# Optimization experiments

Hardware: AMD Instinct MI355X
Metric: run time of the kernel (lower is better)

Reference implementation:

```python
import jax, jax.numpy as jnp
import numpy as np

N_EMBD = 1024
N_HEADS = 16
HEAD_SIZE = N_EMBD // N_HEADS
B, T = 1, 4096
LN_EPS = 1e-5


def setup_inputs() -> dict:
    key = jax.random.key(0)
    ks = jax.random.split(key, 12)
    s = lambda fan_in: 1.0 / np.sqrt(fan_in)
    return {
        "x": jax.random.normal(ks[0], (B, T, N_EMBD), dtype=jnp.float32),
        # per-head Q/K/V projections (no bias), stacked over heads: [H, C, hd]
        "Wq": jax.random.normal(ks[1], (N_HEADS, N_EMBD, HEAD_SIZE), dtype=jnp.float32) * s(N_EMBD),
        "Wk": jax.random.normal(ks[2], (N_HEADS, N_EMBD, HEAD_SIZE), dtype=jnp.float32) * s(N_EMBD),
        "Wv": jax.random.normal(ks[3], (N_HEADS, N_EMBD, HEAD_SIZE), dtype=jnp.float32) * s(N_EMBD),
        # output projection (with bias)
        "Wp": jax.random.normal(ks[4], (N_EMBD, N_EMBD), dtype=jnp.float32) * s(N_EMBD),
        "bp": jnp.zeros((N_EMBD,), dtype=jnp.float32),
        # FFN: Linear(C, 4C) -> ReLU -> Linear(4C, C)
        "W1": jax.random.normal(ks[5], (N_EMBD, 4 * N_EMBD), dtype=jnp.float32) * s(N_EMBD),
        "b1": jnp.zeros((4 * N_EMBD,), dtype=jnp.float32),
        "W2": jax.random.normal(ks[6], (4 * N_EMBD, N_EMBD), dtype=jnp.float32) * s(4 * N_EMBD),
        "b2": jnp.zeros((N_EMBD,), dtype=jnp.float32),
        # LayerNorms
        "g1": jnp.ones((N_EMBD,), dtype=jnp.float32),
        "be1": jnp.zeros((N_EMBD,), dtype=jnp.float32),
        "g2": jnp.ones((N_EMBD,), dtype=jnp.float32),
        "be2": jnp.zeros((N_EMBD,), dtype=jnp.float32),
    }


def _layernorm(x, gamma, beta):
    mu = jnp.mean(x, axis=-1, keepdims=True)
    var = jnp.mean(jnp.square(x - mu), axis=-1, keepdims=True)
    return (x - mu) * jax.lax.rsqrt(var + LN_EPS) * gamma + beta


def _block(x, Wq, Wk, Wv, Wp, bp, W1, b1, W2, b2, g1, be1, g2, be2):
    Bn, Tn, C = x.shape
    h = _layernorm(x, g1, be1)
    # per-head projections: [B, H, T, hd]
    q = jnp.einsum("btc,hcd->bhtd", h, Wq)
    k = jnp.einsum("btc,hcd->bhtd", h, Wk)
    v = jnp.einsum("btc,hcd->bhtd", h, Wv)
    # NOTE: original scales by C**-0.5 where C = n_embd (not head_size)
    scores = jnp.einsum("bhtd,bhsd->bhts", q, k) * (C ** -0.5)
    causal = jnp.tril(jnp.ones((Tn, Tn), dtype=bool))
    scores = jnp.where(causal, scores, -jnp.inf)
    w = jax.nn.softmax(scores, axis=-1)
    attn = jnp.einsum("bhts,bhsd->bhtd", w, v)
    # concat heads: [B, T, H*hd] = [B, T, C]
    attn = attn.transpose(0, 2, 1, 3).reshape(Bn, Tn, C)
    x = x + attn @ Wp + bp
    h2 = _layernorm(x, g2, be2)
    ff = jax.nn.relu(h2 @ W1 + b1) @ W2 + b2
    return x + ff


def reference(x, Wq, Wk, Wv, Wp, bp, W1, b1, W2, b2, g1, be1, g2, be2):
    return _block(x, Wq, Wk, Wv, Wp, bp, W1, b1, W2, b2, g1, be1, g2, be2)
```

## Files before the change

### kernel.cpp

```cpp
#include <hip/hip_runtime.h>
#include <cstdint>

typedef __attribute__((ext_vector_type(8))) short bf16x8;
typedef __attribute__((ext_vector_type(4))) float f32x4;
typedef __attribute__((ext_vector_type(16))) float f32x16;
typedef __attribute__((ext_vector_type(4))) unsigned int u32x4;

__device__ __forceinline__ short f2b(float f) {
  unsigned u = __builtin_bit_cast(unsigned, f);
  unsigned r = (u + 0x7fffu + ((u >> 16) & 1u)) >> 16;
  return (short)(unsigned short)r;
}
__device__ __forceinline__ float b2f(short s) {
  unsigned u = ((unsigned)(unsigned short)s) << 16;
  return __builtin_bit_cast(float, u);
}

__device__ __forceinline__ void gload16(void* lds_dst, const void* gsrc) {
  __builtin_amdgcn_global_load_lds(
      (const __attribute__((address_space(1))) void*)gsrc,
      (__attribute__((address_space(3))) void*)lds_dst, 16, 0, 0);
}

__device__ __forceinline__ unsigned cvtpk(float a, float b) {
  unsigned r;
  asm("v_cvt_pk_bf16_f32 %0, %1, %2" : "=v"(r) : "v"(a), "v"(b));
  return r;
}
__device__ __forceinline__ unsigned shflx32(unsigned v) {
  return (unsigned)__shfl_xor((int)v, 32);
}
__device__ __forceinline__ float exp2x(float x) {
  float r;
  asm("v_exp_f32 %0, %1" : "=v"(r) : "v"(x));
  return r;
}

__device__ __forceinline__ void plswap(unsigned &a, unsigned &b) {
#if __has_builtin(__builtin_amdgcn_permlane32_swap)
  auto r = __builtin_amdgcn_permlane32_swap((int)a, (int)b, false, false);
  a = (unsigned)r[0];
  b = (unsigned)r[1];
#else
  const bool lo = ((threadIdx.x & 63) < 32);
  unsigned ax = shflx32(a), bx = shflx32(b);
  unsigned na = lo ? a : bx;
  unsigned nb = lo ? ax : b;
  a = na; b = nb;
#endif
}

__global__ __launch_bounds__(256)
void prep_all(const float* __restrict__ Wq, const float* __restrict__ Wk,
              const float* __restrict__ Wv, const float* __restrict__ Wp,
              const float* __restrict__ W1, const float* __restrict__ W2,
              const float* __restrict__ x, const float* __restrict__ g1,
              const float* __restrict__ be1,
              short* __restrict__ WqkvT, short* __restrict__ WpT,
              short* __restrict__ W1T, short* __restrict__ W2T,
              short* __restrict__ hbuf)
{
  const int id = blockIdx.x;
  if (id < 12288) {
    __shared__ float tl[32][33];
    const int tx = threadIdx.x & 31;
    const int ty = threadIdx.x >> 5;
    if (id < 3072) {
      const int which = id >> 10;
      const int rem = id & 1023;
      const int head = rem >> 6;
      const int tile = rem & 63;
      const int tc = tile >> 1, td = tile & 1;
      const float* src = (which == 0 ? Wq : which == 1 ? Wk : Wv) + (long)head * 65536;
#pragma unroll
      for (int i2 = 0; i2 < 4; ++i2) {
        int i = ty + i2 * 8;
        tl[i][tx] = src[(long)(tc * 32 + i) * 64 + td * 32 + tx];
      }
      __syncthreads();
      const long base = (long)which * 1024 + head * 64 + td * 32;
#pragma unroll
      for (int i2 = 0; i2 < 4; ++i2) {
        int i = ty + i2 * 8;
        WqkvT[(base + i) * 1024 + tc * 32 + tx] = f2b(tl[tx][i]);
      }
    } else {
      const float* src;
      short* dst;
      int rows, cols, bx, by;
      if (id < 4096) {
        src = Wp; dst = WpT; rows = 1024; cols = 1024;
        const int k = id - 3072; bx = k & 31; by = k >> 5;
      } else if (id < 8192) {
        src = W1; dst = W1T; rows = 1024; cols = 4096;
        const int k = id - 4096; bx = k & 127; by = k >> 7;
      } else {
        src = W2; dst = W2T; rows = 4096; cols = 1024;
        const int k = id - 8192; bx = k & 31; by = k >> 5;
      }
#pragma unroll
      for (int i2 = 0; i2 < 4; ++i2) {
        int i = ty + i2 * 8;
        tl[i][tx] = src[(long)(by * 32 + i) * cols + bx * 32 + tx];
      }
      __syncthreads();
#pragma unroll
      for (int i2 = 0; i2 < 4; ++i2) {
        int i = ty + i2 * 8;
        dst[(long)(bx * 32 + i) * rows + by * 32 + tx] = f2b(tl[tx][i]);
      }
    }
  } else {
    const int row = id - 12288;
    const int t = threadIdx.x;
    const float4 v = ((const float4*)(x + (long)row * 1024))[t];
    float s = v.x + v.y + v.z + v.w;
    float ss = v.x * v.x + v.y * v.y + v.z * v.z + v.w * v.w;
#pragma unroll
    for (int off = 1; off < 64; off <<= 1) {
      s += __shfl_xor(s, off);
      ss += __shfl_xor(ss, off);
    }
    __shared__ float red[8];
    const int wave = t >> 6, lane = t & 63;
    if (lane == 0) { red[wave] = s; red[4 + wave] = ss; }
    __syncthreads();
    s = red[0] + red[1] + red[2] + red[3];
    ss = red[4] + red[5] + red[6] + red[7];
    const float mu = s * (1.f / 1024.f);
    const float rstd = rsqrtf(ss * (1.f / 1024.f) - mu * mu + 1e-5f);
    const float4 gv = ((const float4*)g1)[t];
    const float4 bv = ((const float4*)be1)[t];
    short4 ov;
    ov.x = f2b((v.x - mu) * rstd * gv.x + bv.x);
    ov.y = f2b((v.y - mu) * rstd * gv.y + bv.y);
    ov.z = f2b((v.z - mu) * rstd * gv.z + bv.z);
    ov.w = f2b((v.w - mu) * rstd * gv.w + bv.w);
    *(short4*)(hbuf + (long)row * 1024 + t * 4) = ov;
  }
}

__global__ void vtrans(const short* __restrict__ qkv, short* __restrict__ Vt)
{
  __shared__ short tl[32][33];
  const int t0 = blockIdx.x * 32;
  const int c0 = blockIdx.y * 32;
  const int head = c0 >> 6, d0 = c0 & 63;
  const int tx = threadIdx.x;
#pragma unroll
  for (int i2 = 0; i2 < 4; ++i2) {
    int i = threadIdx.y + i2 * 8;
    tl[i][tx] = qkv[(long)(t0 + i) * 3072 + 2048 + c0 + tx];
  }
  __syncthreads();
#pragma unroll
  for (int i2 = 0; i2 < 4; ++i2) {
    int i = threadIdx.y + i2 * 8;
    Vt[(long)head * 262144 + (long)(d0 + i) * 4096 + t0 + tx] = tl[tx][i];
  }
}

__global__ __launch_bounds__(256)
void layernorm_bf16(const float* __restrict__ x, const float* __restrict__ g,
                    const float* __restrict__ be, short* __restrict__ outp)
{
  const int row = blockIdx.x;
  const int t = threadIdx.x;
  const float4 v = ((const float4*)(x + (long)row * 1024))[t];
  float s = v.x + v.y + v.z + v.w;
  float ss = v.x * v.x + v.y * v.y + v.z * v.z + v.w * v.w;
#pragma unroll
  for (int off = 1; off < 64; off <<= 1) {
    s += __shfl_xor(s, off);
    ss += __shfl_xor(ss, off);
  }
  __shared__ float red[8];
  const int wave = t >> 6, lane = t & 63;
  if (lane == 0) { red[wave] = s; red[4 + wave] = ss; }
  __syncthreads();
  s = red[0] + red[1] + red[2] + red[3];
  ss = red[4] + red[5] + red[6] + red[7];
  const float mu = s * (1.f / 1024.f);
  const float rstd = rsqrtf(ss * (1.f / 1024.f) - mu * mu + 1e-5f);
  const float4 gv = ((const float4*)g)[t];
  const float4 bv = ((const float4*)be)[t];
  short4 ov;
  ov.x = f2b((v.x - mu) * rstd * gv.x + bv.x);
  ov.y = f2b((v.y - mu) * rstd * gv.y + bv.y);
  ov.z = f2b((v.z - mu) * rstd * gv.z + bv.z);
  ov.w = f2b((v.w - mu) * rstd * gv.w + bv.w);
  *(short4*)(outp + (long)row * 1024 + t * 4) = ov;
}

template<int EPI>
__global__ __launch_bounds__(512, 2)
void gemm128(const short* __restrict__ A, const short* __restrict__ Bt,
             int N, int K, int NT,
             short* __restrict__ Cb, float* __restrict__ Cf,
             const float* __restrict__ bias, const float* __restrict__ resid)
{
  __shared__ __align__(16) short As[2 * 8192];
  __shared__ __align__(16) short Bs[2 * 8192];
  const int tid = threadIdx.x;
  const int lane = tid & 63;
  const int wave = tid >> 6;
  const int wm = wave >> 2;
  const int wn = wave & 3;
  const int l15 = lane & 15, lg = lane >> 4;

  const int nwg = gridDim.x * gridDim.y;
  const int lin = blockIdx.y * gridDim.x + blockIdx.x;
  const int swz = (lin & 7) * (nwg >> 3) + (lin >> 3);
  const long m0 = (long)(swz / gridDim.x) * 128;
  const long n0 = (long)(swz % gridDim.x) * 128;

  const int rloc = lane >> 3;
  const int csrc = (lane & 7) ^ rloc;
  const short* Ag = A + (m0 + wave * 8 + rloc) * K + csrc * 8;
  const short* Bg = Bt + (n0 + wave * 8 + rloc) * K + csrc * 8;
  const int wbase = wave * 512;

  f32x4 acc[4][2] = {};

#define STAGE128(buf, kt)                                                     \
  do {                                                                        \
    gload16(As + (buf) * 8192 + wbase, Ag + (kt));                            \
    gload16(As + (buf) * 8192 + 4096 + wbase, Ag + (long)64 * K + (kt));      \
    gload16(Bs + (buf) * 8192 + wbase, Bg + (kt));                            \
    gload16(Bs + (buf) * 8192 + 4096 + wbase, Bg + (long)64 * K + (kt));      \
  } while (0)

  STAGE128(0, 0);
  STAGE128(1, 64);
  asm volatile("s_waitcnt vmcnt(4)" ::: "memory");
  __builtin_amdgcn_sched_barrier(0);
  __builtin_amdgcn_s_barrier();
  __builtin_amdgcn_sched_barrier(0);

  const int cA = l15 & 7;
  for (int t = 0; t < NT; ++t) {
    const char* Ab = (const char*)(As + (t & 1) * 8192);
    const char* Bb = (const char*)(Bs + (t & 1) * 8192);
#pragma unroll
    for (int kk = 0; kk < 2; ++kk) {
      bf16x8 af[4], bk[2];
#pragma unroll
      for (int mi = 0; mi < 4; ++mi)
        af[mi] = *(const bf16x8*)(Ab + (wm * 64 + mi * 16 + l15) * 128 + 16 * ((kk * 4 + lg) ^ cA));
#pragma unroll
      for (int ni = 0; ni < 2; ++ni)
        bk[ni] = *(const bf16x8*)(Bb + (wn * 32 + ni * 16 + l15) * 128 + 16 * ((kk * 4 + lg) ^ cA));
      __builtin_amdgcn_s_setprio(1);
#pragma unroll
      for (int mi = 0; mi < 4; ++mi)
#pragma unroll
        for (int ni = 0; ni < 2; ++ni)
          acc[mi][ni] = __builtin_amdgcn_mfma_f32_16x16x32_bf16(af[mi], bk[ni], acc[mi][ni], 0, 0, 0);
      __builtin_amdgcn_s_setprio(0);
    }
    if (t == NT - 1) break;
    __builtin_amdgcn_s_barrier();
    __builtin_amdgcn_sched_barrier(0);
    if (t + 2 < NT) {
      STAGE128(t & 1, (long)(t + 2) * 64);
      asm volatile("s_waitcnt vmcnt(4)" ::: "memory");
    } else {
      asm volatile("s_waitcnt vmcnt(0)" ::: "memory");
    }
    __builtin_amdgcn_sched_barrier(0);
    __builtin_amdgcn_s_barrier();
    __builtin_amdgcn_sched_barrier(0);
  }
#undef STAGE128

#pragma unroll
  for (int mi = 0; mi < 4; ++mi) {
#pragma unroll
    for (int ni = 0; ni < 2; ++ni) {
      const long col = n0 + wn * 32 + ni * 16 + l15;
#pragma unroll
      for (int r = 0; r < 4; ++r) {
        const long row = m0 + wm * 64 + mi * 16 + lg * 4 + r;
        const long idx = row * N + col;
        float v = acc[mi][ni][r];
        if (EPI == 0) {
          Cb[idx] = f2b(v);
        } else {
          Cf[idx] = v + bias[col] + resid[idx];
        }
      }
    }
  }
}

__device__ __forceinline__ void stage256(short* AsB, short* BsB,
                                         const short* Ag, const short* Bg,
                                         long kt, int K, int ldsoff)
{
#pragma unroll
  for (int p = 0; p < 4; ++p)
    gload16(AsB + p * 4096 + ldsoff, Ag + (long)p * 64 * K + kt);
#pragma unroll
  for (int p = 0; p < 4; ++p)
    gload16(BsB + p * 4096 + ldsoff, Bg + (long)p * 64 * K + kt);
}

template<int EPI>
__global__ __launch_bounds__(512, 2)
void gemm256(const short* __restrict__ A, const short* __restrict__ Bt,
             int N, int K, int NT,
             short* __restrict__ Cb, const float* __restrict__ bias)
{
  __shared__ __align__(16) short As[2 * 16384];
  __shared__ __align__(16) short Bs[2 * 16384];
  const int tid = threadIdx.x;
  const int lane = tid & 63;
  const int wave = tid >> 6;
  const int wm = wave >> 2;
  const int wn = wave & 3;
  const int l15 = lane & 15, lg = lane >> 4;

  const int nwg = gridDim.x * gridDim.y;
  const int lin = blockIdx.y * gridDim.x + blockIdx.x;
  const int swz = (lin & 7) * (nwg >> 3) + (lin >> 3);
  const long m0 = (long)(swz / gridDim.x) * 256;
  const long n0 = (long)(swz % gridDim.x) * 256;

  const int trow = tid >> 3;
  const int csrc = (tid & 7) ^ (trow & 7);
  const short* Ag = A + (m0 + trow) * K + csrc * 8;
  const short* Bg = Bt + (n0 + trow) * K + csrc * 8;
  const int ldsoff = wave * 512;

  f32x4 acc[8][4] = {};

  stage256(As, Bs, Ag, Bg, 0, K, ldsoff);
  asm volatile("s_waitcnt vmcnt(0)" ::: "memory");
  __builtin_amdgcn_sched_barrier(0);
  __builtin_amdgcn_s_barrier();
  __builtin_amdgcn_sched_barrier(0);

  const int cA = l15 & 7;
  for (int t = 0; t < NT; ++t) {
    const char* Ab = (const char*)(As + (t & 1) * 16384);
    const char* Bb = (const char*)(Bs + (t & 1) * 16384);
    short* Asn = As + ((t + 1) & 1) * 16384;
    short* Bsn = Bs + ((t + 1) & 1) * 16384;
    const bool more = (t + 1 < NT);
    const long ktn = (long)(t + 1) * 64;
    bf16x8 bk[4];
#pragma unroll
    for (int ph = 0; ph < 4; ++ph) {
      const int kk = ph >> 1;
      const int mh = (ph & 1) * 4;
      bf16x8 af[4];
#pragma unroll
      for (int mi = 0; mi < 4; ++mi)
        af[mi] = *(const bf16x8*)(Ab + (wm * 128 + (mh + mi) * 16 + l15) * 128 + 16 * ((kk * 4 + lg) ^ cA));
      if ((ph & 1) == 0) {
#pragma unroll
        for (int ni = 0; ni < 4; ++ni)
          bk[ni] = *(const bf16x8*)(Bb + (wn * 64 + ni * 16 + l15) * 128 + 16 * ((kk * 4 + lg) ^ cA));
      }
      if (more && ph == 0) {
#pragma unroll
        for (int p = 0; p < 4; ++p)
          gload16(Asn + p * 4096 + ldsoff, Ag + (long)p * 64 * K + ktn);
      }
      if (more && ph == 1) {
#pragma unroll
        for (int p = 0; p < 4; ++p)
          gload16(Bsn + p * 4096 + ldsoff, Bg + (long)p * 64 * K + ktn);
      }
      __builtin_amdgcn_s_barrier();
      asm volatile("s_waitcnt lgkmcnt(0)" ::: "memory");
      __builtin_amdgcn_sched_barrier(0);
      __builtin_amdgcn_s_setprio(1);
#pragma unroll
      for (int mi = 0; mi < 4; ++mi)
#pragma unroll
        for (int ni = 0; ni < 4; ++ni)
          acc[mh + mi][ni] = __builtin_amdgcn_mfma_f32_16x16x32_bf16(af[mi], bk[ni], acc[mh + mi][ni], 0, 0, 0);
      __builtin_amdgcn_s_setprio(0);
      if (ph == 3 && more) {
        asm volatile("s_waitcnt vmcnt(0)" ::: "memory");
        __builtin_amdgcn_sched_barrier(0);
      }
      __builtin_amdgcn_s_barrier();
      __builtin_amdgcn_sched_barrier(0);
    }
  }

#pragma unroll
  for (int mi = 0; mi < 8; ++mi) {
#pragma unroll
    for (int ni = 0; ni < 4; ++ni) {
      const long col = n0 + wn * 64 + ni * 16 + l15;
      const float bb = (EPI == 2) ? bias[col] : 0.f;
#pragma unroll
      for (int r = 0; r < 4; ++r) {
        const long row = m0 + wm * 128 + mi * 16 + lg * 4 + r;
        float v = acc[mi][ni][r];
        if (EPI == 2) { v += bb; v = v > 0.f ? v : 0.f; }
        Cb[row * N + col] = f2b(v);
      }
    }
  }
}

__device__ __forceinline__ void stage_k32(short* lds, const short* gRowBase)
{
  const int lane = threadIdx.x & 63;
  const int rloc = lane >> 3;
  const int cs = (lane & 7) ^ rloc;
#pragma unroll
  for (int p = 0; p < 4; ++p)
    gload16(lds + p * 512, gRowBase + (long)(p * 8 + rloc) * 3072 + cs * 8);
}
__device__ __forceinline__ void stage_v32(short* lds, const short* vHeadBase, int t0)
{
  const int lane = threadIdx.x & 63;
  const int rloc = lane >> 3;
  const int cs = (lane & 7) ^ rloc;
#pragma unroll
  for (int p = 0; p < 4; ++p) {
    const int row = p * 8 + rloc;
    const int d = row + ((cs & 4) << 3);
    gload16(lds + p * 512, vHeadBase + (long)d * 4096 + t0 + (cs & 3) * 8);
  }
}

__global__ __launch_bounds__(256)
void attn_fwd4(const short* __restrict__ qkv, const short* __restrict__ Vt,
               short* __restrict__ outp)
{
  __shared__ __align__(16) short KV[4 * 8192];
  __shared__ __align__(16) short OB[64 * 64];
  __shared__ float lAll[64];

  const int tid = threadIdx.x;
  const int lane = tid & 63;
  const int wave = tid >> 6;
  const int wq = wave & 1;
  const int ks = wave >> 1;
  const int l31 = lane & 31;
  const int h = lane >> 5;
  const int rs = l31 & 7;

  const int id = blockIdx.x;
  const int head = ((id & 7) << 1) | (id >> 8);
  const int bx = (id >> 3) & 31;

  const short* Qg = qkv + head * 64;
  const short* Kg = qkv + 1024 + head * 64;
  const short* Vg = Vt + (long)head * 262144;

  short* Kw = KV + wave * 8192;

  bf16x8 onesf;
#pragma unroll
  for (int j = 0; j < 8; ++j) onesf[j] = (short)0x3F80;

  for (int ph = 0; ph < 2; ++ph) {
    const int qsuper = ph ? (63 - bx) : bx;
    const int q0 = qsuper * 64 + wq * 32;
    const int q = q0 + l31;
    const int nt = qsuper + 1;

    bf16x8 qf[4];
#pragma unroll
    for (int d = 0; d < 4; ++d) {
      bf16x8 tq = *(const bf16x8*)(Qg + (long)q * 3072 + d * 16 + h * 8);
#pragma unroll
      for (int j = 0; j < 8; ++j) tq[j] = f2b(b2f(tq[j]) * (0.03125f * 1.44269504f));
      qf[d] = tq;
    }

    f32x16 o0 = {}, o1 = {}, lacc = {};

    stage_k32(Kw, Kg + (long)(ks * 32) * 3072);
    stage_v32(Kw + 2048, Vg, ks * 32);
    if (nt > 1) {
      stage_k32(Kw + 4096, Kg + (long)(64 + ks * 32) * 3072);
      stage_v32(Kw + 4096 + 2048, Vg, 64 + ks * 32);
    }

    for (int t = 0; t < nt; ++t) {
      if (t + 1 < nt) {
        asm volatile("s_waitcnt vmcnt(8)" ::: "memory");
      } else {
        asm volatile("s_waitcnt vmcnt(0)" ::: "memory");
      }
      __builtin_amdgcn_sched_barrier(0);
      const char* Kb = (const char*)(Kw + (t & 1) * 4096);
      const char* Vb = Kb + 4096;
      const bf16x8 kf0 = *(const bf16x8*)(Kb + l31 * 128 + 16 * ((0 + h) ^ rs));
      const bf16x8 kf1 = *(const bf16x8*)(Kb + l31 * 128 + 16 * ((2 + h) ^ rs));
      const bf16x8 kf2 = *(const bf16x8*)(Kb + l31 * 128 + 16 * ((4 + h) ^ rs));
      const bf16x8 kf3 = *(const bf16x8*)(Kb + l31 * 128 + 16 * ((6 + h) ^ rs));
      const bf16x8 vf00 = *(const bf16x8*)(Vb + l31 * 128 + 16 * ((0 + h) ^ rs));
      const bf16x8 vf01 = *(const bf16x8*)(Vb + l31 * 128 + 16 * ((2 + h) ^ rs));
      const bf16x8 vf10 = *(const bf16x8*)(Vb + l31 * 128 + 16 * ((4 + h) ^ rs));
      const bf16x8 vf11 = *(const bf16x8*)(Vb + l31 * 128 + 16 * ((6 + h) ^ rs));
      asm volatile("s_waitcnt lgkmcnt(0)" ::: "memory");
      __builtin_amdgcn_sched_barrier(0);
      if (t + 2 < nt) {
        stage_k32(Kw + (t & 1) * 4096, Kg + (long)((t + 2) * 64 + ks * 32) * 3072);
        stage_v32(Kw + (t & 1) * 4096 + 2048, Vg, (t + 2) * 64 + ks * 32);
      }
      f32x16 s = {};
      __builtin_amdgcn_s_setprio(1);
      s = __builtin_amdgcn_mfma_f32_32x32x16_bf16(kf0, qf[0], s, 0, 0, 0);
      s = __builtin_amdgcn_mfma_f32_32x32x16_bf16(kf1, qf[1], s, 0, 0, 0);
      s = __builtin_amdgcn_mfma_f32_32x32x16_bf16(kf2, qf[2], s, 0, 0, 0);
      s = __builtin_amdgcn_mfma_f32_32x32x16_bf16(kf3, qf[3], s, 0, 0, 0);
      __builtin_amdgcn_s_setprio(0);
      if (t == qsuper) {
        const int kb0 = t * 64 + ks * 32 + 4 * h;
#pragma unroll
        for (int r = 0; r < 16; ++r) {
          const int k0 = kb0 + (r & 3) + 8 * (r >> 2);
          if (k0 > q) s[r] = -INFINITY;
        }
      }
#pragma unroll
      for (int r = 0; r < 16; ++r) s[r] = exp2x(s[r]);
      unsigned P0 = cvtpk(s[0], s[1]),   P1 = cvtpk(s[2], s[3]);
      unsigned P2 = cvtpk(s[4], s[5]),   P3 = cvtpk(s[6], s[7]);
      unsigned P4 = cvtpk(s[8], s[9]),   P5 = cvtpk(s[10], s[11]);
      unsigned P6 = cvtpk(s[12], s[13]), P7 = cvtpk(s[14], s[15]);
      plswap(P0, P2); plswap(P1, P3); plswap(P4, P6); plswap(P5, P7);
      u32x4 f0, f1;
      f0[0] = P0; f0[1] = P1; f0[2] = P2; f0[3] = P3;
      f1[0] = P4; f1[1] = P5; f1[2] = P6; f1[3] = P7;
      const bf16x8 pa0 = __builtin_bit_cast(bf16x8, f0);
      const bf16x8 pa1 = __builtin_bit_cast(bf16x8, f1);
      __builtin_amdgcn_s_setprio(1);
      o0 = __builtin_amdgcn_mfma_f32_32x32x16_bf16(pa0, vf00, o0, 0, 0, 0);
      o0 = __builtin_amdgcn_mfma_f32_32x32x16_bf16(pa1, vf01, o0, 0, 0, 0);
      o1 = __builtin_amdgcn_mfma_f32_32x32x16_bf16(pa0, vf10, o1, 0, 0, 0);
      o1 = __builtin_amdgcn_mfma_f32_32x32x16_bf16(pa1, vf11, o1, 0, 0, 0);
      lacc = __builtin_amdgcn_mfma_f32_32x32x16_bf16(pa0, onesf, lacc, 0, 0, 0);
      lacc = __builtin_amdgcn_mfma_f32_32x32x16_bf16(pa1, onesf, lacc, 0, 0, 0);
      __builtin_amdgcn_s_setprio(0);
    }

    if (ks == 1) {
#pragma unroll
      for (int r = 0; r < 16; ++r) {
        const int qq = wq * 32 + (r & 3) + 8 * (r >> 2) + 4 * h;
        OB[qq * 64 + l31] = f2b(o0[r]);
        OB[qq * 64 + 32 + l31] = f2b(o1[r]);
      }
      if (l31 == 0) {
#pragma unroll
        for (int r = 0; r < 16; ++r) {
          const int qq = wq * 32 + (r & 3) + 8 * (r >> 2) + 4 * h;
          lAll[qq] = lacc[r];
        }
      }
    }
    __syncthreads();
    if (ks == 0) {
#pragma unroll
      for (int r = 0; r < 16; ++r) {
        const int qq = wq * 32 + (r & 3) + 8 * (r >> 2) + 4 * h;
        const float inv = 1.f / (lacc[r] + lAll[qq]);
        const long qr = (long)qsuper * 64 + qq;
        const float v0 = o0[r] + b2f(OB[qq * 64 + l31]);
        const float v1 = o1[r] + b2f(OB[qq * 64 + 32 + l31]);
        outp[qr * 1024 + head * 64 + l31] = f2b(v0 * inv);
        outp[qr * 1024 + head * 64 + 32 + l31] = f2b(v1 * inv);
      }
    }
    __syncthreads();
  }
}

extern "C" void kernel_launch(void* const* d_in, const int* in_sizes, int n_in,
                              void* d_out, int out_size, void* d_ws, size_t ws_size,
                              hipStream_t stream)
{
  (void)in_sizes; (void)n_in; (void)out_size; (void)ws_size;
  const float* x   = (const float*)d_in[0];
  const float* Wq  = (const float*)d_in[1];
  const float* Wk  = (const float*)d_in[2];
  const float* Wv  = (const float*)d_in[3];
  const float* Wp  = (const float*)d_in[4];
  const float* bp  = (const float*)d_in[5];
  const float* W1  = (const float*)d_in[6];
  const float* b1  = (const float*)d_in[7];
  const float* W2  = (const float*)d_in[8];
  const float* b2  = (const float*)d_in[9];
  const float* g1  = (const float*)d_in[10];
  const float* be1 = (const float*)d_in[11];
  const float* g2  = (const float*)d_in[12];
  const float* be2 = (const float*)d_in[13];
  float* out = (float*)d_out;

  char* ws = (char*)d_ws;
  const size_t MB = 1ull << 20;
  short* WqkvT = (short*)(ws + 0 * MB);
  short* WpT   = (short*)(ws + 6 * MB);
  short* W1T   = (short*)(ws + 8 * MB);
  short* W2T   = (short*)(ws + 16 * MB);
  short* hbuf  = (short*)(ws + 24 * MB);
  short* qkvb  = (short*)(ws + 32 * MB);
  short* attnb = (short*)(ws + 56 * MB);
  float* x1    = (float*)(ws + 64 * MB);
  short* Vtb   = (short*)(ws + 64 * MB);

  prep_all<<<16384, 256, 0, stream>>>(Wq, Wk, Wv, Wp, W1, W2, x, g1, be1,
                                      WqkvT, WpT, W1T, W2T, hbuf);
  gemm256<0><<<dim3(12, 16), 512, 0, stream>>>(hbuf, WqkvT, 3072, 1024, 16,
                                               qkvb, nullptr);
  vtrans<<<dim3(128, 32), dim3(32, 8), 0, stream>>>(qkvb, Vtb);
  attn_fwd4<<<512, 256, 0, stream>>>(qkvb, Vtb, attnb);
  gemm128<1><<<dim3(8, 32), 512, 0, stream>>>(attnb, WpT, 1024, 1024, 16,
                                              nullptr, x1, bp, x);
  layernorm_bf16<<<4096, 256, 0, stream>>>(x1, g2, be2, hbuf);
  gemm256<2><<<dim3(16, 16), 512, 0, stream>>>(hbuf, W1T, 4096, 1024, 16,
                                               qkvb, b1);
  gemm128<1><<<dim3(8, 32), 512, 0, stream>>>(qkvb, W2T, 1024, 4096, 64,
                                              nullptr, out, b2, x1);
}
```

Before: 248.5 us.

## Replace 256-tile GEMMs with 128-tile kernel and process two KV blocks per attention step

The 256x256-tile gemm256 kernel is removed. The QKV and FFN-up GEMMs now use gemm128, which gains a bias+ReLU epilogue (EPI==2), so those launches get four times as many smaller workgroups for better CU fill. The attention kernel is restructured to consume two 64-key blocks per iteration, with both halves of the LDS buffer refilled together and interleaved MFMA chains. This cuts the number of waits and iterations but changes the prefetch distance, which may expose more memory latency and raise register pressure.

Result: slower. 274.9 us (+10.7%).

```diff
diff --git a/kernel.cpp b/kernel.cpp
--- a/kernel.cpp
+++ b/kernel.cpp
@@ -278,6 +278,7 @@
 #pragma unroll
     for (int ni = 0; ni < 2; ++ni) {
       const long col = n0 + wn * 32 + ni * 16 + l15;
+      const float bb = (EPI == 2) ? bias[col] : 0.f;
 #pragma unroll
       for (int r = 0; r < 4; ++r) {
         const long row = m0 + wm * 64 + mi * 16 + lg * 4 + r;
@@ -285,124 +286,12 @@
         float v = acc[mi][ni][r];
         if (EPI == 0) {
           Cb[idx] = f2b(v);
+        } else if (EPI == 1) {
+          Cf[idx] = v + bias[col] + resid[idx];
         } else {
-          Cf[idx] = v + bias[col] + resid[idx];
+          v += bb;
+          Cb[idx] = f2b(v > 0.f ? v : 0.f);
         }
-      }
-    }
-  }
-}
-
-__device__ __forceinline__ void stage256(short* AsB, short* BsB,
-                                         const short* Ag, const short* Bg,
-                                         long kt, int K, int ldsoff)
-{
-#pragma unroll
-  for (int p = 0; p < 4; ++p)
-    gload16(AsB + p * 4096 + ldsoff, Ag + (long)p * 64 * K + kt);
-#pragma unroll
-  for (int p = 0; p < 4; ++p)
-    gload16(BsB + p * 4096 + ldsoff, Bg + (long)p * 64 * K + kt);
-}
-
-template<int EPI>
-__global__ __launch_bounds__(512, 2)
-void gemm256(const short* __restrict__ A, const short* __restrict__ Bt,
-             int N, int K, int NT,
-             short* __restrict__ Cb, const float* __restrict__ bias)
-{
-  __shared__ __align__(16) short As[2 * 16384];
-  __shared__ __align__(16) short Bs[2 * 16384];
-  const int tid = threadIdx.x;
-  const int lane = tid & 63;
-  const int wave = tid >> 6;
-  const int wm = wave >> 2;
-  const int wn = wave & 3;
-  const int l15 = lane & 15, lg = lane >> 4;
-
-  const int nwg = gridDim.x * gridDim.y;
-  const int lin = blockIdx.y * gridDim.x + blockIdx.x;
-  const int swz = (lin & 7) * (nwg >> 3) + (lin >> 3);
-  const long m0 = (long)(swz / gridDim.x) * 256;
-  const long n0 = (long)(swz % gridDim.x) * 256;
-
-  const int trow = tid >> 3;
-  const int csrc = (tid & 7) ^ (trow & 7);
-  const short* Ag = A + (m0 + trow) * K + csrc * 8;
-  const short* Bg = Bt + (n0 + trow) * K + csrc * 8;
-  const int ldsoff = wave * 512;
-
-  f32x4 acc[8][4] = {};
-
-  stage256(As, Bs, Ag, Bg, 0, K, ldsoff);
-  asm volatile("s_waitcnt vmcnt(0)" ::: "memory");
-  __builtin_amdgcn_sched_barrier(0);
-  __builtin_amdgcn_s_barrier();
-  __builtin_amdgcn_sched_barrier(0);
-
-  const int cA = l15 & 7;
-  for (int t = 0; t < NT; ++t) {
-    const char* Ab = (const char*)(As + (t & 1) * 16384);
-    const char* Bb = (const char*)(Bs + (t & 1) * 16384);
-    short* Asn = As + ((t + 1) & 1) * 16384;
-    short* Bsn = Bs + ((t + 1) & 1) * 16384;
-    const bool more = (t + 1 < NT);
-    const long ktn = (long)(t + 1) * 64;
-    bf16x8 bk[4];
-#pragma unroll
-    for (int ph = 0; ph < 4; ++ph) {
-      const int kk = ph >> 1;
-      const int mh = (ph & 1) * 4;
-      bf16x8 af[4];
-#pragma unroll
-      for (int mi = 0; mi < 4; ++mi)
-        af[mi] = *(const bf16x8*)(Ab + (wm * 128 + (mh + mi) * 16 + l15) * 128 + 16 * ((kk * 4 + lg) ^ cA));
-      if ((ph & 1) == 0) {
-#pragma unroll
-        for (int ni = 0; ni < 4; ++ni)
-          bk[ni] = *(const bf16x8*)(Bb + (wn * 64 + ni * 16 + l15) * 128 + 16 * ((kk * 4 + lg) ^ cA));
-      }
-      if (more && ph == 0) {
-#pragma unroll
-        for (int p = 0; p < 4; ++p)
-          gload16(Asn + p * 4096 + ldsoff, Ag + (long)p * 64 * K + ktn);
-      }
-      if (more && ph == 1) {
-#pragma unroll
-        for (int p = 0; p < 4; ++p)
-          gload16(Bsn + p * 4096 + ldsoff, Bg + (long)p * 64 * K + ktn);
-      }
-      __builtin_amdgcn_s_barrier();
-      asm volatile("s_waitcnt lgkmcnt(0)" ::: "memory");
-      __builtin_amdgcn_sched_barrier(0);
-      __builtin_amdgcn_s_setprio(1);
-#pragma unroll
-      for (int mi = 0; mi < 4; ++mi)
-#pragma unroll
-        for (int ni = 0; ni < 4; ++ni)
-          acc[mh + mi][ni] = __builtin_amdgcn_mfma_f32_16x16x32_bf16(af[mi], bk[ni], acc[mh + mi][ni], 0, 0, 0);
-      __builtin_amdgcn_s_setprio(0);
-      if (ph == 3 && more) {
-        asm volatile("s_waitcnt vmcnt(0)" ::: "memory");
-        __builtin_amdgcn_sched_barrier(0);
-      }
-      __builtin_amdgcn_s_barrier();
-      __builtin_amdgcn_sched_barrier(0);
-    }
-  }
-
-#pragma unroll
-  for (int mi = 0; mi < 8; ++mi) {
-#pragma unroll
-    for (int ni = 0; ni < 4; ++ni) {
-      const long col = n0 + wn * 64 + ni * 16 + l15;
-      const float bb = (EPI == 2) ? bias[col] : 0.f;
-#pragma unroll
-      for (int r = 0; r < 4; ++r) {
-        const long row = m0 + wm * 128 + mi * 16 + lg * 4 + r;
-        float v = acc[mi][ni][r];
-        if (EPI == 2) { v += bb; v = v > 0.f ? v : 0.f; }
-        Cb[row * N + col] = f2b(v);
       }
     }
   }
@@ -431,7 +320,7 @@
 }
 
 __global__ __launch_bounds__(256)
-void attn_fwd4(const short* __restrict__ qkv, const short* __restrict__ Vt,
+void attn_fwd5(const short* __restrict__ qkv, const short* __restrict__ Vt,
                short* __restrict__ outp)
 {
   __shared__ __align__(16) short KV[4 * 8192];
@@ -482,66 +371,152 @@
     stage_v32(Kw + 2048, Vg, ks * 32);
     if (nt > 1) {
       stage_k32(Kw + 4096, Kg + (long)(64 + ks * 32) * 3072);
-      stage_v32(Kw + 4096 + 2048, Vg, 64 + ks * 32);
-    }
-
-    for (int t = 0; t < nt; ++t) {
-      if (t + 1 < nt) {
-        asm volatile("s_waitcnt vmcnt(8)" ::: "memory");
-      } else {
-        asm volatile("s_waitcnt vmcnt(0)" ::: "memory");
-      }
+      stage_v32(Kw + 6144, Vg, 64 + ks * 32);
+    }
+
+    int t = 0;
+    for (; t + 1 < nt; t += 2) {
+      asm volatile("s_waitcnt vmcnt(0)" ::: "memory");
       __builtin_amdgcn_sched_barrier(0);
-      const char* Kb = (const char*)(Kw + (t & 1) * 4096);
-      const char* Vb = Kb + 4096;
-      const bf16x8 kf0 = *(const bf16x8*)(Kb + l31 * 128 + 16 * ((0 + h) ^ rs));
-      const bf16x8 kf1 = *(const bf16x8*)(Kb + l31 * 128 + 16 * ((2 + h) ^ rs));
-      const bf16x8 kf2 = *(const bf16x8*)(Kb + l31 * 128 + 16 * ((4 + h) ^ rs));
-      const bf16x8 kf3 = *(const bf16x8*)(Kb + l31 * 128 + 16 * ((6 + h) ^ rs));
-      const bf16x8 vf00 = *(const bf16x8*)(Vb + l31 * 128 + 16 * ((0 + h) ^ rs));
-      const bf16x8 vf01 = *(const bf16x8*)(Vb + l31 * 128 + 16 * ((2 + h) ^ rs));
-      const bf16x8 vf10 = *(const bf16x8*)(Vb + l31 * 128 + 16 * ((4 + h) ^ rs));
-      const bf16x8 vf11 = *(const bf16x8*)(Vb + l31 * 128 + 16 * ((6 + h) ^ rs));
+      const char* Kb0 = (const char*)Kw;
+      const char* Vb0 = Kb0 + 4096;
+      const char* Kb1 = Kb0 + 8192;
+      const char* Vb1 = Kb0 + 12288;
+      bf16x8 k0f[4], k1f[4], v0f[4], v1f[4];
+#pragma unroll
+      for (int c = 0; c < 4; ++c) {
+        k0f[c] = *(const bf16x8*)(Kb0 + l31 * 128 + 16 * ((2 * c + h) ^ rs));
+        k1f[c] = *(const bf16x8*)(Kb1 + l31 * 128 + 16 * ((2 * c + h) ^ rs));
+      }
+#pragma unroll
+      for (int c = 0; c < 4; ++c) {
+        v0f[c] = *(const bf16x8*)(Vb0 + l31 * 128 + 16 * ((2 * c + h) ^ rs));
+        v1f[c] = *(const bf16x8*)(Vb1 + l31 * 128 + 16 * ((2 * c + h) ^ rs));
+      }
       asm volatile("s_waitcnt lgkmcnt(0)" ::: "memory");
       __builtin_amdgcn_sched_barrier(0);
-      if (t + 2 < nt) {
-        stage_k32(Kw + (t & 1) * 4096, Kg + (long)((t + 2) * 64 + ks * 32) * 3072);
-        stage_v32(Kw + (t & 1) * 4096 + 2048, Vg, (t + 2) * 64 + ks * 32);
-      }
-      f32x16 s = {};
+      if (t + 3 < nt) {
+        stage_k32(Kw, Kg + (long)((t + 2) * 64 + ks * 32) * 3072);
+        stage_v32(Kw + 2048, Vg, (t + 2) * 64 + ks * 32);
+        stage_k32(Kw + 4096, Kg + (long)((t + 3) * 64 + ks * 32) * 3072);
+        stage_v32(Kw + 6144, Vg, (t + 3) * 64 + ks * 32);
+      } else if (t + 2 < nt) {
+        stage_k32(Kw, Kg + (long)((t + 2) * 64 + ks * 32) * 3072);
+        stage_v32(Kw + 2048, Vg, (t + 2) * 64 + ks * 32);
+      }
+      f32x16 sA = {}, sB = {};
       __builtin_amdgcn_s_setprio(1);
-      s = __builtin_amdgcn_mfma_f32_32x32x16_bf16(kf0, qf[0], s, 0, 0, 0);
-      s = __builtin_amdgcn_mfma_f32_32x32x16_bf16(kf1, qf[1], s, 0, 0, 0);
-      s = __builtin_amdgcn_mfma_f32_32x32x16_bf16(kf2, qf[2], s, 0, 0, 0);
-      s = __builtin_amdgcn_mfma_f32_32x32x16_bf16(kf3, qf[3], s, 0, 0, 0);
+      sA = __builtin_amdgcn_mfma_f32_32x32x16_bf16(k0f[0], qf[0], sA, 0, 0, 0);
+      sB = __builtin_amdgcn_mfma_f32_32x32x16_bf16(k1f[0], qf[0], sB, 0, 0, 0);
+      sA = __builtin_amdgcn_mfma_f32_32x32x16_bf16(k0f[1], qf[1], sA, 0, 0, 0);
+      sB = __builtin_amdgcn_mfma_f32_32x32x16_bf16(k1f[1], qf[1], sB, 0, 0, 0);
+      sA = __builtin_amdgcn_mfma_f32_32x32x16_bf16(k0f[2], qf[2], sA, 0, 0, 0);
+      sB = __builtin_amdgcn_mfma_f32_32x32x16_bf16(k1f[2], qf[2], sB, 0, 0, 0);
+      sA = __builtin_amdgcn_mfma_f32_32x32x16_bf16(k0f[3], qf[3], sA, 0, 0, 0);
+      sB = __builtin_amdgcn_mfma_f32_32x32x16_bf16(k1f[3], qf[3], sB, 0, 0, 0);
       __builtin_amdgcn_s_setprio(0);
       if (t == qsuper) {
         const int kb0 = t * 64 + ks * 32 + 4 * h;
 #pragma unroll
         for (int r = 0; r < 16; ++r) {
           const int k0 = kb0 + (r & 3) + 8 * (r >> 2);
-          if (k0 > q) s[r] = -INFINITY;
+          if (k0 > q) sA[r] = -INFINITY;
         }
       }
-#pragma unroll
-      for (int r = 0; r < 16; ++r) s[r] = exp2x(s[r]);
-      unsigned P0 = cvtpk(s[0], s[1]),   P1 = cvtpk(s[2], s[3]);
-      unsigned P2 = cvtpk(s[4], s[5]),   P3 = cvtpk(s[6], s[7]);
-      unsigned P4 = cvtpk(s[8], s[9]),   P5 = cvtpk(s[10], s[11]);
-      unsigned P6 = cvtpk(s[12], s[13]), P7 = cvtpk(s[14], s[15]);
-      plswap(P0, P2); plswap(P1, P3); plswap(P4, P6); plswap(P5, P7);
-      u32x4 f0, f1;
-      f0[0] = P0; f0[1] = P1; f0[2] = P2; f0[3] = P3;
-      f1[0] = P4; f1[1] = P5; f1[2] = P6; f1[3] = P7;
-      const bf16x8 pa0 = __builtin_bit_cast(bf16x8, f0);
-      const bf16x8 pa1 = __builtin_bit_cast(bf16x8, f1);
+      if (t + 1 == qsuper) {
+        const int kb1 = (t + 1) * 64 + ks * 32 + 4 * h;
+#pragma unroll
+        for (int r = 0; r < 16; ++r) {
+          const int k1 = kb1 + (r & 3) + 8 * (r >> 2);
+          if (k1 > q) sB[r] = -INFINITY;
+        }
+      }
+#pragma unroll
+      for (int r = 0; r < 16; ++r) {
+        sA[r] = exp2x(sA[r]);
+        sB[r] = exp2x(sB[r]);
+      }
+      unsigned A0 = cvtpk(sA[0], sA[1]),   A1 = cvtpk(sA[2], sA[3]);
+      unsigned A2 = cvtpk(sA[4], sA[5]),   A3 = cvtpk(sA[6], sA[7]);
+      unsigned A4 = cvtpk(sA[8], sA[9]),   A5 = cvtpk(sA[10], sA[11]);
+      unsigned A6 = cvtpk(sA[12], sA[13]), A7 = cvtpk(sA[14], sA[15]);
+      unsigned B0 = cvtpk(sB[0], sB[1]),   B1 = cvtpk(sB[2], sB[3]);
+      unsigned B2 = cvtpk(sB[4], sB[5]),   B3 = cvtpk(sB[6], sB[7]);
+      unsigned B4 = cvtpk(sB[8], sB[9]),   B5 = cvtpk(sB[10], sB[11]);
+      unsigned B6 = cvtpk(sB[12], sB[13]), B7 = cvtpk(sB[14], sB[15]);
+      plswap(A0, A2); plswap(A1, A3); plswap(A4, A6); plswap(A5, A7);
+      plswap(B0, B2); plswap(B1, B3); plswap(B4, B6); plswap(B5, B7);
+      u32x4 fa0, fa1, fb0, fb1;
+      fa0[0] = A0; fa0[1] = A1; fa0[2] = A2; fa0[3] = A3;
+      fa1[0] = A4; fa1[1] = A5; fa1[2] = A6; fa1[3] = A7;
+      fb0[0] = B0; fb0[1] = B1; fb0[2] = B2; fb0[3] = B3;
+      fb1[0] = B4; fb1[1] = B5; fb1[2] = B6; fb1[3] = B7;
+      const bf16x8 paA0 = __builtin_bit_cast(bf16x8, fa0);
+      const bf16x8 paA1 = __builtin_bit_cast(bf16x8, fa1);
+      const bf16x8 paB0 = __builtin_bit_cast(bf16x8, fb0);
+      const bf16x8 paB1 = __builtin_bit_cast(bf16x8, fb1);
       __builtin_amdgcn_s_setprio(1);
-      o0 = __builtin_amdgcn_mfma_f32_32x32x16_bf16(pa0, vf00, o0, 0, 0, 0);
-      o0 = __builtin_amdgcn_mfma_f32_32x32x16_bf16(pa1, vf01, o0, 0, 0, 0);
-      o1 = __builtin_amdgcn_mfma_f32_32x32x16_bf16(pa0, vf10, o1, 0, 0, 0);
-      o1 = __builtin_amdgcn_mfma_f32_32x32x16_bf16(pa1, vf11, o1, 0, 0, 0);
-      lacc = __builtin_amdgcn_mfma_f32_32x32x16_bf16(pa0, onesf, lacc, 0, 0, 0);
-      lacc = __builtin_amdgcn_mfma_f32_32x32x16_bf16(pa1, onesf, lacc, 0, 0, 0);
+      o0 = __builtin_amdgcn_mfma_f32_32x32x16_bf16(paA0, v0f[0], o0, 0, 0, 0);
+      o1 = __builtin_amdgcn_mfma_f32_32x32x16_bf16(paA0, v0f[2], o1, 0, 0, 0);
+      lacc = __builtin_amdgcn_mfma_f32_32x32x16_bf16(paA0, onesf, lacc, 0, 0, 0);
+      o0 = __builtin_amdgcn_mfma_f32_32x32x16_bf16(paA1, v0f[1], o0, 0, 0, 0);
+      o1 = __builtin_amdgcn_mfma_f32_32x32x16_bf16(paA1, v0f[3], o1, 0, 0, 0);
+      lacc = __builtin_amdgcn_mfma_f32_32x32x16_bf16(paA1, onesf, lacc, 0, 0, 0);
+      o0 = __builtin_amdgcn_mfma_f32_32x32x16_bf16(paB0, v1f[0], o0, 0, 0, 0);
+      o1 = __builtin_amdgcn_mfma_f32_32x32x16_bf16(paB0, v1f[2], o1, 0, 0, 0);
+      lacc = __builtin_amdgcn_mfma_f32_32x32x16_bf16(paB0, onesf, lacc, 0, 0, 0);
+      o0 = __builtin_amdgcn_mfma_f32_32x32x16_bf16(paB1, v1f[1], o0, 0, 0, 0);
+      o1 = __builtin_amdgcn_mfma_f32_32x32x16_bf16(paB1, v1f[3], o1, 0, 0, 0);
+      lacc = __builtin_amdgcn_mfma_f32_32x32x16_bf16(paB1, onesf, lacc, 0, 0, 0);
+      __builtin_amdgcn_s_setprio(0);
+    }
+    if (t < nt) {
+      asm volatile("s_waitcnt vmcnt(0)" ::: "memory");
+      __builtin_amdgcn_sched_barrier(0);
+      const char* Kb0 = (const char*)Kw;
+      const char* Vb0 = Kb0 + 4096;
+      bf16x8 k0f[4], v0f[4];
+#pragma unroll
+      for (int c = 0; c < 4; ++c) {
+        k0f[c] = *(const bf16x8*)(Kb0 + l31 * 128 + 16 * ((2 * c + h) ^ rs));
+        v0f[c] = *(const bf16x8*)(Vb0 + l31 * 128 + 16 * ((2 * c + h) ^ rs));
+      }
+      asm volatile("s_waitcnt lgkmcnt(0)" ::: "memory");
+      __builtin_amdgcn_sched_barrier(0);
+      f32x16 sA = {};
+      __builtin_amdgcn_s_setprio(1);
+      sA = __builtin_amdgcn_mfma_f32_32x32x16_bf16(k0f[0], qf[0], sA, 0, 0, 0);
+      sA = __builtin_amdgcn_mfma_f32_32x32x16_bf16(k0f[1], qf[1], sA, 0, 0, 0);
+      sA = __builtin_amdgcn_mfma_f32_32x32x16_bf16(k0f[2], qf[2], sA, 0, 0, 0);
+      sA = __builtin_amdgcn_mfma_f32_32x32x16_bf16(k0f[3], qf[3], sA, 0, 0, 0);
+      __builtin_amdgcn_s_setprio(0);
+      if (t == qsuper) {
+        const int kb0 = t * 64 + ks * 32 + 4 * h;
+#pragma unroll
+        for (int r = 0; r < 16; ++r) {
+          const int k0 = kb0 + (r & 3) + 8 * (r >> 2);
+          if (k0 > q) sA[r] = -INFINITY;
+        }
+      }
+#pragma unroll
+      for (int r = 0; r < 16; ++r) sA[r] = exp2x(sA[r]);
+      unsigned A0 = cvtpk(sA[0], sA[1]),   A1 = cvtpk(sA[2], sA[3]);
+      unsigned A2 = cvtpk(sA[4], sA[5]),   A3 = cvtpk(sA[6], sA[7]);
+      unsigned A4 = cvtpk(sA[8], sA[9]),   A5 = cvtpk(sA[10], sA[11]);
+      unsigned A6 = cvtpk(sA[12], sA[13]), A7 = cvtpk(sA[14], sA[15]);
+      plswap(A0, A2); plswap(A1, A3); plswap(A4, A6); plswap(A5, A7);
+      u32x4 fa0, fa1;
+      fa0[0] = A0; fa0[1] = A1; fa0[2] = A2; fa0[3] = A3;
+      fa1[0] = A4; fa1[1] = A5; fa1[2] = A6; fa1[3] = A7;
+      const bf16x8 paA0 = __builtin_bit_cast(bf16x8, fa0);
+      const bf16x8 paA1 = __builtin_bit_cast(bf16x8, fa1);
+      __builtin_amdgcn_s_setprio(1);
+      o0 = __builtin_amdgcn_mfma_f32_32x32x16_bf16(paA0, v0f[0], o0, 0, 0, 0);
+      o1 = __builtin_amdgcn_mfma_f32_32x32x16_bf16(paA0, v0f[2], o1, 0, 0, 0);
+      lacc = __builtin_amdgcn_mfma_f32_32x32x16_bf16(paA0, onesf, lacc, 0, 0, 0);
+      o0 = __builtin_amdgcn_mfma_f32_32x32x16_bf16(paA1, v0f[1], o0, 0, 0, 0);
+      o1 = __builtin_amdgcn_mfma_f32_32x32x16_bf16(paA1, v0f[3], o1, 0, 0, 0);
+      lacc = __builtin_amdgcn_mfma_f32_32x32x16_bf16(paA1, onesf, lacc, 0, 0, 0);
       __builtin_amdgcn_s_setprio(0);
     }
 
@@ -612,15 +587,15 @@
 
   prep_all<<<16384, 256, 0, stream>>>(Wq, Wk, Wv, Wp, W1, W2, x, g1, be1,
                                       WqkvT, WpT, W1T, W2T, hbuf);
-  gemm256<0><<<dim3(12, 16), 512, 0, stream>>>(hbuf, WqkvT, 3072, 1024, 16,
-                                               qkvb, nullptr);
+  gemm128<0><<<dim3(24, 32), 512, 0, stream>>>(hbuf, WqkvT, 3072, 1024, 16,
+                                               qkvb, nullptr, nullptr, nullptr);
   vtrans<<<dim3(128, 32), dim3(32, 8), 0, stream>>>(qkvb, Vtb);
-  attn_fwd4<<<512, 256, 0, stream>>>(qkvb, Vtb, attnb);
+  attn_fwd5<<<512, 256, 0, stream>>>(qkvb, Vtb, attnb);
   gemm128<1><<<dim3(8, 32), 512, 0, stream>>>(attnb, WpT, 1024, 1024, 16,
                                               nullptr, x1, bp, x);
   layernorm_bf16<<<4096, 256, 0, stream>>>(x1, g2, be2, hbuf);
-  gemm256<2><<<dim3(16, 16), 512, 0, stream>>>(hbuf, W1T, 4096, 1024, 16,
-                                               qkvb, b1);
+  gemm128<2><<<dim3(32, 32), 512, 0, stream>>>(hbuf, W1T, 4096, 1024, 16,
+                                               qkvb, nullptr, b1, nullptr);
   gemm128<1><<<dim3(8, 32), 512, 0, stream>>>(qkvb, W2T, 1024, 4096, 64,
                                               nullptr, out, b2, x1);
 }
```
